# Kernel optimization log

Hardware: AMD Instinct MI355X
Metric: run time of the kernel (lower is better)

The kernel has to match this reference:

```python
import jax, jax.numpy as jnp
import numpy as np

N_QUBITS = 16
N_BLOCKS = 8
N_ADDR_QUBITS = 4  # (8).bit_length() -> min(n_qubits, bit_length)
N_HEADS = 16


def setup_inputs() -> dict:
    key = jax.random.key(0)
    ks = jax.random.split(key, 9)
    B, S, D, M, J, Q = 4, 2048, 1024, 2048, N_BLOCKS, N_QUBITS
    s = lambda d: 1.0 / np.sqrt(d)
    return {
        "query": jax.random.normal(ks[0], (B, S, D), jnp.float32),
        "W_addr": jax.random.normal(ks[1], (D, Q), jnp.float32) * s(D),
        "b_addr": jnp.zeros((Q,), jnp.float32),
        "memory": jax.random.normal(ks[2], (J, M), jnp.float32),
        "W_out": jax.random.normal(ks[3], (M, D), jnp.float32) * s(M),
        "b_out": jnp.zeros((D,), jnp.float32),
        "Wq": jax.random.normal(ks[4], (D, D), jnp.float32) * s(D),
        "bq": jnp.zeros((D,), jnp.float32),
        "Wk": jax.random.normal(ks[5], (D, D), jnp.float32) * s(D),
        "bk": jnp.zeros((D,), jnp.float32),
        "Wv": jax.random.normal(ks[6], (D, D), jnp.float32) * s(D),
        "bv": jnp.zeros((D,), jnp.float32),
        "Wo": jax.random.normal(ks[7], (D, D), jnp.float32) * s(D),
        "bo": jnp.zeros((D,), jnp.float32),
    }


def _address_weights(query, W_addr, b_addr):
    # Deterministic expectation of the per-token quantum register loop:
    # RX(theta) applied iff theta > 0 -> P(measure 1) = sin^2(theta/2), else 0.
    theta = query @ W_addr + b_addr                      # [B,S,Q]
    p1 = jnp.where(theta > 0, jnp.sin(theta * 0.5) ** 2, 0.0)
    p = p1[..., :N_ADDR_QUBITS]                          # only bit_length(J) qubits used
    bits = ((jnp.arange(N_BLOCKS)[:, None] >> jnp.arange(N_ADDR_QUBITS)[None, :]) & 1
            ).astype(query.dtype)                        # [J, Qa]
    # score[b,s,j] = sum_q [ bits*p + (1-bits)*(1-p) ]
    scores = jnp.einsum("bsq,jq->bsj", p, bits) + jnp.einsum("bsq,jq->bsj", 1.0 - p, 1.0 - bits)
    return jax.nn.softmax(scores, axis=-1)               # [B,S,J]


def reference(query, W_addr, b_addr, memory, W_out, b_out,
              Wq, bq, Wk, bk, Wv, bv, Wo, bo):
    addr = _address_weights(query, W_addr, b_addr)       # [B,S,J]
    mem_read = jnp.einsum("bsj,jm->bsm", addr, memory)   # [B,S,M]
    out = mem_read @ W_out + b_out                       # [B,S,D]

    # quantum_attention(q=k=v=out): multi-head self-attention
    B, S, D = out.shape
    hd = D // N_HEADS
    q = (out @ Wq + bq).reshape(B, S, N_HEADS, hd)
    k = (out @ Wk + bk).reshape(B, S, N_HEADS, hd)
    v = (out @ Wv + bv).reshape(B, S, N_HEADS, hd)
    att = jax.nn.softmax(jnp.einsum("bihd,bjhd->bhij", q, k) / np.sqrt(hd), axis=-1)
    ctx = jnp.einsum("bhij,bjhd->bihd", att, v).reshape(B, S, D)
    return ctx @ Wo + bo
```

## Files before the change

kernel.cpp:

```cpp
#include <hip/hip_runtime.h>

#define B_ 4
#define S_ 2048
#define D_ 1024
#define M_ 2048
#define J_ 8
#define H_ 16
#define HD_ 64
#define BH_ 64

typedef __attribute__((ext_vector_type(8))) short short8;
typedef __attribute__((ext_vector_type(4))) float f32x4;
typedef __attribute__((ext_vector_type(16))) float f32x16;

static __device__ __forceinline__ unsigned short f2bf(float x) {
  unsigned u = __float_as_uint(x);
  u = u + 0x7fffu + ((u >> 16) & 1u);
  return (unsigned short)(u >> 16);
}

static __device__ __forceinline__ unsigned cvtpk(float lo, float hi) {
  unsigned r;
  asm("v_cvt_pk_bf16_f32 %0, %1, %2" : "=v"(r) : "v"(lo), "v"(hi));
  return r;
}

static __device__ __forceinline__ void gload16(const void* g, void* l) {
  __builtin_amdgcn_global_load_lds(
      (const __attribute__((address_space(1))) unsigned*)g,
      (__attribute__((address_space(3))) unsigned*)l, 16, 0, 0);
}

__global__ __launch_bounds__(256) void k_mw_part(const float* __restrict__ memory,
                                                 const float* __restrict__ W_out,
                                                 float* __restrict__ part) {
  int nc = blockIdx.x >> 4, ks = blockIdx.x & 15;
  int t = threadIdx.x;
  int n = nc * 64 + (t & 63);
  int sub = t >> 6;
  int k0 = ks * 128 + sub * 32;
  float acc[J_];
#pragma unroll
  for (int j = 0; j < J_; ++j) acc[j] = 0.f;
  for (int k = k0; k < k0 + 32; ++k) {
    float wv = W_out[(size_t)k * D_ + n];
#pragma unroll
    for (int j = 0; j < J_; ++j) acc[j] += memory[j * M_ + k] * wv;
  }
  __shared__ float p4[4][J_][64];
#pragma unroll
  for (int j = 0; j < J_; ++j) p4[sub][j][t & 63] = acc[j];
  __syncthreads();
  if (t < 64) {
#pragma unroll
    for (int j = 0; j < J_; ++j)
      part[((size_t)ks * J_ + j) * D_ + nc * 64 + t] =
          p4[0][j][t] + p4[1][j][t] + p4[2][j][t] + p4[3][j][t];
  }
}

__global__ __launch_bounds__(256) void k_mw_red(const float* __restrict__ part,
                                                const float* __restrict__ b_out,
                                                float* __restrict__ G) {
  int id = blockIdx.x * 256 + threadIdx.x;
  int j = id >> 10, n = id & 1023;
  if (j < 8) {
    float s = 0.f;
#pragma unroll
    for (int ks = 0; ks < 16; ++ks) s += part[((size_t)ks * J_ + j) * D_ + n];
    G[j * D_ + n] = s;
  } else {
    G[8 * D_ + n] = b_out[n];
  }
}

__global__ __launch_bounds__(256) void k_mwq_part(const float* __restrict__ G,
                                                  const float* __restrict__ Wq,
                                                  const float* __restrict__ Wk,
                                                  const float* __restrict__ Wv,
                                                  float* __restrict__ partq) {
  int wi = blockIdx.x >> 6;
  int r = blockIdx.x & 63;
  int nc = r & 15, ks = r >> 4;
  const float* W = wi == 0 ? Wq : (wi == 1 ? Wk : Wv);
  int t = threadIdx.x;
  int n = nc * 64 + (t & 63);
  int sub = t >> 6;
  int k0 = ks * 256 + sub * 64;
  float acc[9];
#pragma unroll
  for (int j = 0; j < 9; ++j) acc[j] = 0.f;
  for (int k = k0; k < k0 + 64; ++k) {
    float wv = W[(size_t)k * D_ + n];
#pragma unroll
    for (int j = 0; j < 9; ++j) acc[j] += G[j * D_ + k] * wv;
  }
  __shared__ float p4[4][9][64];
#pragma unroll
  for (int j = 0; j < 9; ++j) p4[sub][j][t & 63] = acc[j];
  __syncthreads();
  if (t < 64) {
#pragma unroll
    for (int j = 0; j < 9; ++j)
      partq[(((size_t)wi * 4 + ks) * 9 + j) * D_ + nc * 64 + t] =
          p4[0][j][t] + p4[1][j][t] + p4[2][j][t] + p4[3][j][t];
  }
}

__global__ __launch_bounds__(256) void k_mwq_red(const float* __restrict__ partq,
                                                 float* __restrict__ Hq,
                                                 float* __restrict__ Hk,
                                                 float* __restrict__ Hv) {
  int id = blockIdx.x * 256 + threadIdx.x;
  int wi = id / 9216;
  int rem = id - wi * 9216;
  int j = rem >> 10, n = rem & 1023;
  float s = 0.f;
#pragma unroll
  for (int ks = 0; ks < 4; ++ks)
    s += partq[(((size_t)wi * 4 + ks) * 9 + j) * D_ + n];
  float* Hh = wi == 0 ? Hq : (wi == 1 ? Hk : Hv);
  Hh[j * D_ + n] = s;
}

__global__ __launch_bounds__(256) void k_wot(const float* __restrict__ Wo,
                                             unsigned short* __restrict__ WoT) {
  int kt = blockIdx.x, nt = blockIdx.y;
  int t = threadIdx.x;
  __shared__ float tl[64][65];
  int r = t >> 6, c = t & 63;
#pragma unroll
  for (int i = 0; i < 16; ++i) {
    int row = i * 4 + r;
    tl[row][c] = Wo[(size_t)(kt * 64 + row) * D_ + nt * 64 + c];
  }
  __syncthreads();
#pragma unroll
  for (int i = 0; i < 16; ++i) {
    int nrow = i * 4 + r;
    WoT[(size_t)(nt * 64 + nrow) * D_ + kt * 64 + c] = f2bf(tl[c][nrow]);
  }
}

__global__ __launch_bounds__(256) void k_qkv(
    const float* __restrict__ query, const float* __restrict__ W_addr,
    const float* __restrict__ b_addr, const float* __restrict__ Hq,
    const float* __restrict__ Hk, const float* __restrict__ Hv,
    const float* __restrict__ bq, const float* __restrict__ bk,
    const float* __restrict__ bv, unsigned short* __restrict__ Qg,
    unsigned short* __restrict__ Kg, unsigned short* __restrict__ Vg) {
  int w = threadIdx.x >> 6, l = threadIdx.x & 63;
  int tk = blockIdx.x * 4 + w;
  int b = tk >> 11, s = tk & (S_ - 1);
  const float* qrow = query + (size_t)tk * D_;
  float th0 = 0.f, th1 = 0.f, th2 = 0.f, th3 = 0.f;
#pragma unroll
  for (int e = 0; e < 4; ++e) {
    float4 qv = *(const float4*)(qrow + l * 16 + e * 4);
    float xs[4] = {qv.x, qv.y, qv.z, qv.w};
#pragma unroll
    for (int kk = 0; kk < 4; ++kk) {
      float4 wr = *(const float4*)(W_addr + (size_t)(l * 16 + e * 4 + kk) * 16);
      th0 += xs[kk] * wr.x;
      th1 += xs[kk] * wr.y;
      th2 += xs[kk] * wr.z;
      th3 += xs[kk] * wr.w;
    }
  }
#pragma unroll
  for (int off = 32; off; off >>= 1) {
    th0 += __shfl_xor(th0, off);
    th1 += __shfl_xor(th1, off);
    th2 += __shfl_xor(th2, off);
    th3 += __shfl_xor(th3, off);
  }
  float thv[4] = {th0 + b_addr[0], th1 + b_addr[1], th2 + b_addr[2],
                  th3 + b_addr[3]};
  float p[4];
#pragma unroll
  for (int q = 0; q < 4; ++q) {
    float sh = __sinf(thv[q] * 0.5f);
    p[q] = thv[q] > 0.f ? sh * sh : 0.f;
  }
  float sc[8];
  float mx = -1e30f;
#pragma unroll
  for (int j = 0; j < 8; ++j) {
    float v = 0.f;
#pragma unroll
    for (int q = 0; q < 4; ++q) v += ((j >> q) & 1) ? p[q] : 1.f - p[q];
    sc[j] = v;
    mx = fmaxf(mx, v);
  }
  float sum = 0.f;
#pragma unroll
  for (int j = 0; j < 8; ++j) {
    sc[j] = __expf(sc[j] - mx);
    sum += sc[j];
  }
  float inv = 1.f / sum;
  float a[8];
#pragma unroll
  for (int j = 0; j < 8; ++j) a[j] = sc[j] * inv;

  const float* Hs[3] = {Hq, Hk, Hv};
  const float* bs[3] = {bq, bk, bv};
  unsigned short* os[3] = {Qg, Kg, Vg};
#pragma unroll
  for (int k = 0; k < 4; ++k) {
    int n0 = k * 256 + l * 4;
    int hh = n0 >> 6, d = n0 & 63;
    size_t obase = ((size_t)(b * H_ + hh) * S_ + s) * HD_ + d;
#pragma unroll
    for (int wi = 0; wi < 3; ++wi) {
      const float* Hh = Hs[wi];
      float4 accv = *(const float4*)(Hh + 8 * D_ + n0);
      float4 bias = *(const float4*)(bs[wi] + n0);
      accv.x += bias.x; accv.y += bias.y; accv.z += bias.z; accv.w += bias.w;
#pragma unroll
      for (int j = 0; j < 8; ++j) {
        float4 hv = *(const float4*)(Hh + j * D_ + n0);
        accv.x += a[j] * hv.x;
        accv.y += a[j] * hv.y;
        accv.z += a[j] * hv.z;
        accv.w += a[j] * hv.w;
      }
      uint2 pk;
      pk.x = (unsigned)f2bf(accv.x) | ((unsigned)f2bf(accv.y) << 16);
      pk.y = (unsigned)f2bf(accv.z) | ((unsigned)f2bf(accv.w) << 16);
      *(uint2*)(os[wi] + obase) = pk;
    }
  }
}

__global__ __launch_bounds__(256) void k_vt(const unsigned short* __restrict__ Vg,
                                            unsigned short* __restrict__ Vtg) {
  int st = blockIdx.x & 31, bh = blockIdx.x >> 5;
  int t = threadIdx.x;
  __shared__ unsigned short tl[64][65];
  int rr = t >> 3, c8 = t & 7;
#pragma unroll
  for (int p = 0; p < 2; ++p) {
    int s = p * 32 + rr;
    uint4 v = *(const uint4*)(Vg + ((size_t)bh * S_ + st * 64 + s) * HD_ + c8 * 8);
    const unsigned short* pv = (const unsigned short*)&v;
#pragma unroll
    for (int j = 0; j < 8; ++j) tl[s][c8 * 8 + j] = pv[j];
  }
  __syncthreads();
#pragma unroll
  for (int p = 0; p < 2; ++p) {
    int d = p * 32 + rr;
    unsigned short o[8];
#pragma unroll
    for (int j = 0; j < 8; ++j) o[j] = tl[c8 * 8 + j][d];
    *(uint4*)(Vtg + ((size_t)bh * HD_ + d) * S_ + st * 64 + c8 * 8) = *(const uint4*)o;
  }
}

__global__ __launch_bounds__(512, 4) void k_attn(
    const unsigned short* __restrict__ Qg, const unsigned short* __restrict__ Kg,
    const unsigned short* __restrict__ Vtg, unsigned short* __restrict__ ctxg) {
  int id = blockIdx.x;
  int xcd = id & 7;
  int qt = (id >> 3) & 15;
  int bh = xcd * 8 + (id >> 7);
  int t = threadIdx.x;
  int w = t >> 6, l = t & 63;
  int q31 = l & 31, h = l >> 5;
  int g = w >> 2;

  __shared__ __align__(16) unsigned short lds[32768];

  int q0 = qt * 128;
  const unsigned short* qp = Qg + ((size_t)bh * S_ + q0 + (w & 3) * 32 + q31) * HD_;
  short8 qf0 = *(const short8*)(qp + 0 + h * 8);
  short8 qf1 = *(const short8*)(qp + 16 + h * 8);
  short8 qf2 = *(const short8*)(qp + 32 + h * 8);
  short8 qf3 = *(const short8*)(qp + 48 + h * 8);

  f32x16 accO0 = {}, accO1 = {};
  float lsum = 0.f;

  const unsigned short* kgb = Kg + (size_t)bh * S_ * HD_;
  const unsigned short* vtb = Vtg + (size_t)bh * HD_ * S_;
  int wg = w & 3;
  int rowK = l >> 3, gsl = l & 7;
  int srcg = gsl ^ rowK;

  {
    unsigned short* sKd = lds + g * 8192;
    unsigned short* sVd = sKd + 4096;
#pragma unroll
    for (int cc = 0; cc < 2; ++cc) {
      int c = wg * 2 + cc;
      int rr = c * 8 + rowK;
      gload16(kgb + ((size_t)(g * 1024 + rr)) * HD_ + srcg * 8, sKd + c * 512);
      gload16(vtb + (size_t)rr * S_ + g * 1024 + srcg * 8, sVd + c * 512);
    }
  }
  __syncthreads();

  const float K1 = 0.125f * 1.44269504f;
  const float M2 = 28.8539008f;

  for (int it = 0; it < 16; ++it) {
    if (it < 15) {
      int kvn = g * 1024 + (it + 1) * 64;
      unsigned short* sKd = lds + ((it + 1) & 1) * 16384 + g * 8192;
      unsigned short* sVd = sKd + 4096;
#pragma unroll
      for (int cc = 0; cc < 2; ++cc) {
        int c = wg * 2 + cc;
        int rr = c * 8 + rowK;
        gload16(kgb + (size_t)(kvn + rr) * HD_ + srcg * 8, sKd + c * 512);
        gload16(vtb + (size_t)rr * S_ + kvn + srcg * 8, sVd + c * 512);
      }
    }
    unsigned short* sK = lds + (it & 1) * 16384 + g * 8192;
    unsigned short* sVt = sK + 4096;

    f32x16 accS0 = {}, accS1 = {};
    __builtin_amdgcn_s_setprio(1);
#pragma unroll
    for (int ds = 0; ds < 4; ++ds) {
      short8 qq = ds == 0 ? qf0 : ds == 1 ? qf1 : ds == 2 ? qf2 : qf3;
      {
        int row = q31;
        int gk = (ds * 2 + h) ^ (row & 7);
        short8 kf = *(const short8*)(sK + row * 64 + gk * 8);
        accS0 = __builtin_amdgcn_mfma_f32_32x32x16_bf16(kf, qq, accS0, 0, 0, 0);
      }
      {
        int row = 32 + q31;
        int gk = (ds * 2 + h) ^ (row & 7);
        short8 kf = *(const short8*)(sK + row * 64 + gk * 8);
        accS1 = __builtin_amdgcn_mfma_f32_32x32x16_bf16(kf, qq, accS1, 0, 0, 0);
      }
    }
    __builtin_amdgcn_s_setprio(0);

    float ts = 0.f;
#pragma unroll
    for (int r = 0; r < 16; ++r) {
      float p0 = __builtin_exp2f(accS0[r] * K1 - M2);
      float p1 = __builtin_exp2f(accS1[r] * K1 - M2);
      accS0[r] = p0;
      accS1[r] = p1;
      ts += p0 + p1;
    }
    lsum += ts;

    short8 pb[4];
#pragma unroll
    for (int ks = 0; ks < 4; ++ks) {
      const int r0 = 8 * (ks & 1);
      float v0, v1, v2, v3, v4, v5, v6, v7;
      if (ks < 2) {
        v0 = accS0[r0 + 0]; v1 = accS0[r0 + 1]; v2 = accS0[r0 + 2]; v3 = accS0[r0 + 3];
        v4 = accS0[r0 + 4]; v5 = accS0[r0 + 5]; v6 = accS0[r0 + 6]; v7 = accS0[r0 + 7];
      } else {
        v0 = accS1[r0 + 0]; v1 = accS1[r0 + 1]; v2 = accS1[r0 + 2]; v3 = accS1[r0 + 3];
        v4 = accS1[r0 + 4]; v5 = accS1[r0 + 5]; v6 = accS1[r0 + 6]; v7 = accS1[r0 + 7];
      }
      unsigned X0 = cvtpk(v0, v1), X1 = cvtpk(v2, v3);
      unsigned Y0 = cvtpk(v4, v5), Y1 = cvtpk(v6, v7);
      union { unsigned u[4]; short8 s8; } uu;
#if __has_builtin(__builtin_amdgcn_permlane32_swap)
      typedef __attribute__((ext_vector_type(2))) unsigned uint2v;
      uint2v r02 = __builtin_amdgcn_permlane32_swap(X0, Y0, false, false);
      uint2v r13 = __builtin_amdgcn_permlane32_swap(X1, Y1, false, false);
      uu.u[0] = r02[0]; uu.u[1] = r13[0]; uu.u[2] = r02[1]; uu.u[3] = r13[1];
#else
      unsigned tX0 = __shfl_xor(X0, 32), tX1 = __shfl_xor(X1, 32);
      unsigned tY0 = __shfl_xor(Y0, 32), tY1 = __shfl_xor(Y1, 32);
      uu.u[0] = h ? tY0 : X0;
      uu.u[1] = h ? tY1 : X1;
      uu.u[2] = h ? Y0 : tX0;
      uu.u[3] = h ? Y1 : tX1;
#endif
      pb[ks] = uu.s8;
    }

    __builtin_amdgcn_s_setprio(1);
    {
      int row = q31;
      int rs = row & 7;
#pragma unroll
      for (int ks = 0; ks < 4; ++ks) {
        int gv = (ks * 2 + h) ^ rs;
        short8 vf = *(const short8*)(sVt + row * 64 + gv * 8);
        accO0 = __builtin_amdgcn_mfma_f32_32x32x16_bf16(vf, pb[ks], accO0, 0, 0, 0);
      }
    }
    {
      int row = 32 + q31;
      int rs = row & 7;
#pragma unroll
      for (int ks = 0; ks < 4; ++ks) {
        int gv = (ks * 2 + h) ^ rs;
        short8 vf = *(const short8*)(sVt + row * 64 + gv * 8);
        accO1 = __builtin_amdgcn_mfma_f32_32x32x16_bf16(vf, pb[ks], accO1, 0, 0, 0);
      }
    }
    __builtin_amdgcn_s_setprio(0);

    __syncthreads();
  }

  float lt = lsum + __shfl_xor(lsum, 32);

  if (g == 1) {
    unsigned* xO = (unsigned*)lds;
    int base = ((w & 3) * 64 + l) * 17;
#pragma unroll
    for (int j = 0; j < 8; ++j) xO[base + j] = cvtpk(accO0[2 * j], accO0[2 * j + 1]);
#pragma unroll
    for (int j = 0; j < 8; ++j) xO[base + 8 + j] = cvtpk(accO1[2 * j], accO1[2 * j + 1]);
    float* xml = (float*)(lds + 8704);
    if (h == 0) xml[(w & 3) * 32 + q31] = lt;
  }
  __syncthreads();
  float inv = 0.f;
  if (g == 0) {
    unsigned* xO = (unsigned*)lds;
    float* xml = (float*)(lds + 8704);
    int base = (w * 64 + l) * 17;
    inv = 1.f / (lt + xml[w * 32 + q31]);
#pragma unroll
    for (int j = 0; j < 8; ++j) {
      unsigned wd = xO[base + j];
      accO0[2 * j] += __uint_as_float(wd << 16);
      accO0[2 * j + 1] += __uint_as_float(wd & 0xffff0000u);
    }
#pragma unroll
    for (int j = 0; j < 8; ++j) {
      unsigned wd = xO[base + 8 + j];
      accO1[2 * j] += __uint_as_float(wd << 16);
      accO1[2 * j + 1] += __uint_as_float(wd & 0xffff0000u);
    }
  }
  __syncthreads();
  if (g == 0) {
    int row = w * 32 + q31;
    int swz = (q31 & 7) << 3;
#pragma unroll
    for (int r = 0; r < 16; ++r) {
      int dl = (r & 3) + 8 * (r >> 2) + 4 * h;
      lds[row * 64 + (dl ^ swz)] = f2bf(accO0[r] * inv);
      lds[row * 64 + ((32 + dl) ^ swz)] = f2bf(accO1[r] * inv);
    }
  }
  __syncthreads();
  int b = bh >> 4, head = bh & 15;
#pragma unroll
  for (int j = 0; j < 2; ++j) {
    int slot = t + j * 512;
    int row = slot >> 3, gg = slot & 7;
    uint4 vv = *(const uint4*)(lds + row * 64 + ((gg ^ (row & 7)) * 8));
    *(uint4*)(ctxg + ((size_t)(b * S_ + q0 + row)) * D_ + head * HD_ + gg * 8) = vv;
  }
}

__global__ __launch_bounds__(256) void k_out(const unsigned short* __restrict__ Ag,
                                             const unsigned short* __restrict__ Btg,
                                             const float* __restrict__ bo,
                                             float* __restrict__ out) {
  int mt = blockIdx.x;
  int nt = blockIdx.y;
  int t = threadIdx.x;
  int w = t >> 6, l = t & 63;
  int l15 = l & 15, l4 = l >> 4;
  int wr = w >> 1, wc = w & 1;
  __shared__ __align__(16) unsigned short sA[128 * 64];
  __shared__ __align__(16) unsigned short sB[128 * 64];
  f32x4 acc[4][4];
#pragma unroll
  for (int mm = 0; mm < 4; ++mm)
#pragma unroll
    for (int nn = 0; nn < 4; ++nn) acc[mm][nn] = (f32x4){0.f, 0.f, 0.f, 0.f};
  int srow = t >> 3, sc8 = t & 7;
  for (int kt = 0; kt < 16; ++kt) {
    int k0 = kt * 64;
    __syncthreads();
#pragma unroll
    for (int p = 0; p < 4; ++p) {
      int row = p * 32 + srow;
      int di = row * 64 + ((sc8 * 8) ^ ((row & 7) << 3));
      *(uint4*)(sA + di) =
          *(const uint4*)(Ag + (size_t)(mt * 128 + row) * D_ + k0 + sc8 * 8);
      *(uint4*)(sB + di) =
          *(const uint4*)(Btg + (size_t)(nt * 128 + row) * D_ + k0 + sc8 * 8);
    }
    __syncthreads();
    short8 a[4][2];
#pragma unroll
    for (int mm = 0; mm < 4; ++mm) {
      int row = wr * 64 + mm * 16 + l15;
      int sw = (row & 7) << 3;
      a[mm][0] = *(const short8*)(sA + row * 64 + ((l4 * 8) ^ sw));
      a[mm][1] = *(const short8*)(sA + row * 64 + ((32 + l4 * 8) ^ sw));
    }
#pragma unroll
    for (int nn = 0; nn < 4; ++nn) {
      int row = wc * 64 + nn * 16 + l15;
      int sw = (row & 7) << 3;
      short8 b0 = *(const short8*)(sB + row * 64 + ((l4 * 8) ^ sw));
      short8 b1 = *(const short8*)(sB + row * 64 + ((32 + l4 * 8) ^ sw));
#pragma unroll
      for (int mm = 0; mm < 4; ++mm) {
        acc[mm][nn] = __builtin_amdgcn_mfma_f32_16x16x32_bf16(a[mm][0], b0, acc[mm][nn], 0, 0, 0);
        acc[mm][nn] = __builtin_amdgcn_mfma_f32_16x16x32_bf16(a[mm][1], b1, acc[mm][nn], 0, 0, 0);
      }
    }
  }
#pragma unroll
  for (int mm = 0; mm < 4; ++mm) {
#pragma unroll
    for (int r = 0; r < 4; ++r) {
      int mrow = mt * 128 + wr * 64 + mm * 16 + l4 * 4 + r;
      float* orow = out + (size_t)mrow * D_ + nt * 128 + wc * 64;
#pragma unroll
      for (int nn = 0; nn < 4; ++nn) {
        int n = nn * 16 + l15;
        orow[n] = acc[mm][nn][r] + bo[nt * 128 + wc * 64 + n];
      }
    }
  }
}

extern "C" void kernel_launch(void* const* d_in, const int* in_sizes, int n_in,
                              void* d_out, int out_size, void* d_ws, size_t ws_size,
                              hipStream_t stream) {
  const float* query = (const float*)d_in[0];
  const float* W_addr = (const float*)d_in[1];
  const float* b_addr = (const float*)d_in[2];
  const float* memory = (const float*)d_in[3];
  const float* W_out = (const float*)d_in[4];
  const float* b_out = (const float*)d_in[5];
  const float* Wq = (const float*)d_in[6];
  const float* bq = (const float*)d_in[7];
  const float* Wk = (const float*)d_in[8];
  const float* bk = (const float*)d_in[9];
  const float* Wv = (const float*)d_in[10];
  const float* bv = (const float*)d_in[11];
  const float* Wo = (const float*)d_in[12];
  const float* bo = (const float*)d_in[13];
  float* out = (float*)d_out;

  char* ws = (char*)d_ws;
  size_t off = 0;
  auto alloc = [&](size_t bytes) {
    char* p = ws + off;
    off = (off + bytes + 255) & ~(size_t)255;
    return p;
  };
  float* G = (float*)alloc(9 * D_ * sizeof(float));
  float* HqA = (float*)alloc(9 * D_ * sizeof(float));
  float* HkA = (float*)alloc(9 * D_ * sizeof(float));
  float* HvA = (float*)alloc(9 * D_ * sizeof(float));
  float* partmw = (float*)alloc(16 * J_ * D_ * sizeof(float));
  float* partq = (float*)alloc(3 * 4 * 9 * D_ * sizeof(float));
  unsigned short* WoT = (unsigned short*)alloc((size_t)D_ * D_ * 2);
  unsigned short* Vg = (unsigned short*)alloc((size_t)BH_ * S_ * HD_ * 2);
  unsigned short* Vtg = (unsigned short*)alloc((size_t)BH_ * S_ * HD_ * 2);
  unsigned short* Qg = (unsigned short*)d_out;
  unsigned short* Kg = Qg + (size_t)BH_ * S_ * HD_;
  unsigned short* ctx = Vg;

  k_mw_part<<<256, 256, 0, stream>>>(memory, W_out, partmw);
  k_mw_red<<<36, 256, 0, stream>>>(partmw, b_out, G);
  k_mwq_part<<<192, 256, 0, stream>>>(G, Wq, Wk, Wv, partq);
  k_mwq_red<<<108, 256, 0, stream>>>(partq, HqA, HkA, HvA);
  k_wot<<<dim3(16, 16), 256, 0, stream>>>(Wo, WoT);
  k_qkv<<<B_ * S_ / 4, 256, 0, stream>>>(query, W_addr, b_addr, HqA, HkA, HvA,
                                         bq, bk, bv, Qg, Kg, Vg);
  k_vt<<<BH_ * 32, 256, 0, stream>>>(Vg, Vtg);
  k_attn<<<1024, 512, 0, stream>>>(Qg, Kg, Vtg, ctx);
  k_out<<<dim3(64, 8), 256, 0, stream>>>(ctx, WoT, bo, out);
}
```

Measured before the change: 241.0 us.

## Stage QKV projection tables in LDS as bf16, fold biases and softmax scale

Transposes W_addr for coalesced theta loads and folds the q/k/v biases into the H tables, with the attention scale and log2e pre-multiplied into Hq. k_qkv now stages all three H tables as packed bf16 in shared memory and processes 32 tokens per 512-thread block, writing 16 contiguous outputs per lane. The attention kernel initialises its score accumulators with the max offset so the per-element multiply-subtract before exp2 disappears. This trades some precision (bf16 H tables, a pre-scaled Q) for less global traffic and fewer ALU ops in both kernels.

New measurement: 484.4 us. +101.0%, slower.

```diff
diff --git a/kernel.cpp b/kernel.cpp
--- a/kernel.cpp
+++ b/kernel.cpp
@@ -12,6 +12,9 @@
 typedef __attribute__((ext_vector_type(8))) short short8;
 typedef __attribute__((ext_vector_type(4))) float f32x4;
 typedef __attribute__((ext_vector_type(16))) float f32x16;
+
+#define QSCALE 0.18033688f
+#define M2F 28.8539008f
 
 static __device__ __forceinline__ unsigned short f2bf(float x) {
   unsigned u = __float_as_uint(x);
@@ -61,7 +64,16 @@
 
 __global__ __launch_bounds__(256) void k_mw_red(const float* __restrict__ part,
                                                 const float* __restrict__ b_out,
-                                                float* __restrict__ G) {
+                                                const float* __restrict__ W_addr,
+                                                float* __restrict__ G,
+                                                float* __restrict__ WaT) {
+  if (blockIdx.x >= 36) {
+    int q = blockIdx.x - 36;
+    int c = threadIdx.x * 4;
+#pragma unroll
+    for (int e = 0; e < 4; ++e) WaT[q * D_ + c + e] = W_addr[(size_t)(c + e) * 16 + q];
+    return;
+  }
   int id = blockIdx.x * 256 + threadIdx.x;
   int j = id >> 10, n = id & 1023;
   if (j < 8) {
@@ -108,6 +120,9 @@
 }
 
 __global__ __launch_bounds__(256) void k_mwq_red(const float* __restrict__ partq,
+                                                 const float* __restrict__ bq,
+                                                 const float* __restrict__ bk,
+                                                 const float* __restrict__ bv,
                                                  float* __restrict__ Hq,
                                                  float* __restrict__ Hk,
                                                  float* __restrict__ Hv) {
@@ -119,6 +134,8 @@
 #pragma unroll
   for (int ks = 0; ks < 4; ++ks)
     s += partq[(((size_t)wi * 4 + ks) * 9 + j) * D_ + n];
+  if (j == 8) s += wi == 0 ? bq[n] : (wi == 1 ? bk[n] : bv[n]);
+  if (wi == 0) s *= QSCALE;
   float* Hh = wi == 0 ? Hq : (wi == 1 ? Hk : Hv);
   Hh[j * D_ + n] = s;
 }
@@ -142,93 +159,110 @@
   }
 }
 
-__global__ __launch_bounds__(256) void k_qkv(
-    const float* __restrict__ query, const float* __restrict__ W_addr,
+__global__ __launch_bounds__(512) void k_qkv(
+    const float* __restrict__ query, const float* __restrict__ WaT,
     const float* __restrict__ b_addr, const float* __restrict__ Hq,
     const float* __restrict__ Hk, const float* __restrict__ Hv,
-    const float* __restrict__ bq, const float* __restrict__ bk,
-    const float* __restrict__ bv, unsigned short* __restrict__ Qg,
-    unsigned short* __restrict__ Kg, unsigned short* __restrict__ Vg) {
-  int w = threadIdx.x >> 6, l = threadIdx.x & 63;
-  int tk = blockIdx.x * 4 + w;
-  int b = tk >> 11, s = tk & (S_ - 1);
-  const float* qrow = query + (size_t)tk * D_;
-  float th0 = 0.f, th1 = 0.f, th2 = 0.f, th3 = 0.f;
-#pragma unroll
-  for (int e = 0; e < 4; ++e) {
-    float4 qv = *(const float4*)(qrow + l * 16 + e * 4);
-    float xs[4] = {qv.x, qv.y, qv.z, qv.w};
-#pragma unroll
-    for (int kk = 0; kk < 4; ++kk) {
-      float4 wr = *(const float4*)(W_addr + (size_t)(l * 16 + e * 4 + kk) * 16);
-      th0 += xs[kk] * wr.x;
-      th1 += xs[kk] * wr.y;
-      th2 += xs[kk] * wr.z;
-      th3 += xs[kk] * wr.w;
-    }
-  }
-#pragma unroll
-  for (int off = 32; off; off >>= 1) {
-    th0 += __shfl_xor(th0, off);
-    th1 += __shfl_xor(th1, off);
-    th2 += __shfl_xor(th2, off);
-    th3 += __shfl_xor(th3, off);
-  }
-  float thv[4] = {th0 + b_addr[0], th1 + b_addr[1], th2 + b_addr[2],
-                  th3 + b_addr[3]};
-  float p[4];
-#pragma unroll
-  for (int q = 0; q < 4; ++q) {
-    float sh = __sinf(thv[q] * 0.5f);
-    p[q] = thv[q] > 0.f ? sh * sh : 0.f;
-  }
-  float sc[8];
-  float mx = -1e30f;
-#pragma unroll
-  for (int j = 0; j < 8; ++j) {
-    float v = 0.f;
-#pragma unroll
-    for (int q = 0; q < 4; ++q) v += ((j >> q) & 1) ? p[q] : 1.f - p[q];
-    sc[j] = v;
-    mx = fmaxf(mx, v);
-  }
-  float sum = 0.f;
-#pragma unroll
-  for (int j = 0; j < 8; ++j) {
-    sc[j] = __expf(sc[j] - mx);
-    sum += sc[j];
-  }
-  float inv = 1.f / sum;
-  float a[8];
-#pragma unroll
-  for (int j = 0; j < 8; ++j) a[j] = sc[j] * inv;
-
+    unsigned short* __restrict__ Qg, unsigned short* __restrict__ Kg,
+    unsigned short* __restrict__ Vg) {
+  __shared__ unsigned HL[13824];
+  int t = threadIdx.x;
   const float* Hs[3] = {Hq, Hk, Hv};
-  const float* bs[3] = {bq, bk, bv};
-  unsigned short* os[3] = {Qg, Kg, Vg};
-#pragma unroll
-  for (int k = 0; k < 4; ++k) {
-    int n0 = k * 256 + l * 4;
-    int hh = n0 >> 6, d = n0 & 63;
-    size_t obase = ((size_t)(b * H_ + hh) * S_ + s) * HD_ + d;
-#pragma unroll
-    for (int wi = 0; wi < 3; ++wi) {
-      const float* Hh = Hs[wi];
-      float4 accv = *(const float4*)(Hh + 8 * D_ + n0);
-      float4 bias = *(const float4*)(bs[wi] + n0);
-      accv.x += bias.x; accv.y += bias.y; accv.z += bias.z; accv.w += bias.w;
+#pragma unroll
+  for (int i = 0; i < 27; ++i) {
+    int fid = i * 512 + t;
+    int mat = fid / 4608;
+    int rem = fid - mat * 4608;
+    int row = rem >> 9, cp = rem & 511;
+    float2 v = *(const float2*)(Hs[mat] + (size_t)row * D_ + cp * 2);
+    HL[fid] = cvtpk(v.x, v.y);
+  }
+  __syncthreads();
+
+  int w = t >> 6, l = t & 63;
+  float ba0 = b_addr[0], ba1 = b_addr[1], ba2 = b_addr[2], ba3 = b_addr[3];
+  for (int rd = 0; rd < 4; ++rd) {
+    int tk = blockIdx.x * 32 + rd * 8 + w;
+    int b = tk >> 11, s = tk & (S_ - 1);
+    const float* qrow = query + (size_t)tk * D_;
+    float th0 = 0.f, th1 = 0.f, th2 = 0.f, th3 = 0.f;
+#pragma unroll
+    for (int e = 0; e < 4; ++e) {
+      float4 qv = *(const float4*)(qrow + l * 16 + e * 4);
+      float4 w0 = *(const float4*)(WaT + 0 * D_ + l * 16 + e * 4);
+      float4 w1 = *(const float4*)(WaT + 1 * D_ + l * 16 + e * 4);
+      float4 w2 = *(const float4*)(WaT + 2 * D_ + l * 16 + e * 4);
+      float4 w3 = *(const float4*)(WaT + 3 * D_ + l * 16 + e * 4);
+      th0 += qv.x * w0.x + qv.y * w0.y + qv.z * w0.z + qv.w * w0.w;
+      th1 += qv.x * w1.x + qv.y * w1.y + qv.z * w1.z + qv.w * w1.w;
+      th2 += qv.x * w2.x + qv.y * w2.y + qv.z * w2.z + qv.w * w2.w;
+      th3 += qv.x * w3.x + qv.y * w3.y + qv.z * w3.z + qv.w * w3.w;
+    }
+#pragma unroll
+    for (int off = 32; off; off >>= 1) {
+      th0 += __shfl_xor(th0, off);
+      th1 += __shfl_xor(th1, off);
+      th2 += __shfl_xor(th2, off);
+      th3 += __shfl_xor(th3, off);
+    }
+    float thv[4] = {th0 + ba0, th1 + ba1, th2 + ba2, th3 + ba3};
+    float p[4];
+#pragma unroll
+    for (int q = 0; q < 4; ++q) {
+      float sh = __sinf(thv[q] * 0.5f);
+      p[q] = thv[q] > 0.f ? sh * sh : 0.f;
+    }
+    float sc[8];
+    float mx = -1e30f;
+#pragma unroll
+    for (int j = 0; j < 8; ++j) {
+      float v = 0.f;
+#pragma unroll
+      for (int q = 0; q < 4; ++q) v += ((j >> q) & 1) ? p[q] : 1.f - p[q];
+      sc[j] = v;
+      mx = fmaxf(mx, v);
+    }
+    float sum = 0.f;
+#pragma unroll
+    for (int j = 0; j < 8; ++j) {
+      sc[j] = __expf(sc[j] - mx);
+      sum += sc[j];
+    }
+    float inv = 1.f / sum;
+    float a[8];
+#pragma unroll
+    for (int j = 0; j < 8; ++j) a[j] = sc[j] * inv;
+
+    int head = l >> 2, d0 = (l & 3) * 16;
+    size_t obase = ((size_t)(b * H_ + head) * S_ + s) * HD_ + d0;
+    unsigned short* os[3] = {Qg, Kg, Vg};
+#pragma unroll
+    for (int mat = 0; mat < 3; ++mat) {
+      const unsigned* hb = HL + mat * 4608;
+      float acc[16];
+#pragma unroll
+      for (int c = 0; c < 8; ++c) {
+        unsigned wd = hb[8 * 512 + 8 * l + c];
+        acc[2 * c] = __uint_as_float(wd << 16);
+        acc[2 * c + 1] = __uint_as_float(wd & 0xffff0000u);
+      }
 #pragma unroll
       for (int j = 0; j < 8; ++j) {
-        float4 hv = *(const float4*)(Hh + j * D_ + n0);
-        accv.x += a[j] * hv.x;
-        accv.y += a[j] * hv.y;
-        accv.z += a[j] * hv.z;
-        accv.w += a[j] * hv.w;
-      }
-      uint2 pk;
-      pk.x = (unsigned)f2bf(accv.x) | ((unsigned)f2bf(accv.y) << 16);
-      pk.y = (unsigned)f2bf(accv.z) | ((unsigned)f2bf(accv.w) << 16);
-      *(uint2*)(os[wi] + obase) = pk;
+        float aj = a[j];
+        const unsigned* hr = hb + j * 512 + 8 * l;
+#pragma unroll
+        for (int c = 0; c < 8; ++c) {
+          unsigned wd = hr[c];
+          acc[2 * c] += aj * __uint_as_float(wd << 16);
+          acc[2 * c + 1] += aj * __uint_as_float(wd & 0xffff0000u);
+        }
+      }
+      unsigned ow[8];
+#pragma unroll
+      for (int c = 0; c < 8; ++c) ow[c] = (unsigned)f2bf(acc[2 * c]) |
+                                          ((unsigned)f2bf(acc[2 * c + 1]) << 16);
+      *(uint4*)(os[mat] + obase) = *(const uint4*)&ow[0];
+      *(uint4*)(os[mat] + obase + 8) = *(const uint4*)&ow[4];
     }
   }
 }
@@ -301,9 +335,6 @@
   }
   __syncthreads();
 
-  const float K1 = 0.125f * 1.44269504f;
-  const float M2 = 28.8539008f;
-
   for (int it = 0; it < 16; ++it) {
     if (it < 15) {
       int kvn = g * 1024 + (it + 1) * 64;
@@ -320,7 +351,9 @@
     unsigned short* sK = lds + (it & 1) * 16384 + g * 8192;
     unsigned short* sVt = sK + 4096;
 
-    f32x16 accS0 = {}, accS1 = {};
+    f32x16 accS0, accS1;
+#pragma unroll
+    for (int r = 0; r < 16; ++r) { accS0[r] = -M2F; accS1[r] = -M2F; }
     __builtin_amdgcn_s_setprio(1);
 #pragma unroll
     for (int ds = 0; ds < 4; ++ds) {
@@ -343,8 +376,8 @@
     float ts = 0.f;
 #pragma unroll
     for (int r = 0; r < 16; ++r) {
-      float p0 = __builtin_exp2f(accS0[r] * K1 - M2);
-      float p1 = __builtin_exp2f(accS1[r] * K1 - M2);
+      float p0 = __builtin_exp2f(accS0[r]);
+      float p1 = __builtin_exp2f(accS1[r]);
       accS0[r] = p0;
       accS1[r] = p1;
       ts += p0 + p1;
@@ -559,6 +592,7 @@
   float* HqA = (float*)alloc(9 * D_ * sizeof(float));
   float* HkA = (float*)alloc(9 * D_ * sizeof(float));
   float* HvA = (float*)alloc(9 * D_ * sizeof(float));
+  float* WaT = (float*)alloc(4 * D_ * sizeof(float));
   float* partmw = (float*)alloc(16 * J_ * D_ * sizeof(float));
   float* partq = (float*)alloc(3 * 4 * 9 * D_ * sizeof(float));
   unsigned short* WoT = (unsigned short*)alloc((size_t)D_ * D_ * 2);
@@ -569,12 +603,11 @@
   unsigned short* ctx = Vg;
 
   k_mw_part<<<256, 256, 0, stream>>>(memory, W_out, partmw);
-  k_mw_red<<<36, 256, 0, stream>>>(partmw, b_out, G);
+  k_mw_red<<<40, 256, 0, stream>>>(partmw, b_out, W_addr, G, WaT);
   k_mwq_part<<<192, 256, 0, stream>>>(G, Wq, Wk, Wv, partq);
-  k_mwq_red<<<108, 256, 0, stream>>>(partq, HqA, HkA, HvA);
+  k_mwq_red<<<108, 256, 0, stream>>>(partq, bq, bk, bv, HqA, HkA, HvA);
   k_wot<<<dim3(16, 16), 256, 0, stream>>>(Wo, WoT);
-  k_qkv<<<B_ * S_ / 4, 256, 0, stream>>>(query, W_addr, b_addr, HqA, HkA, HvA,
-                                         bq, bk, bv, Qg, Kg, Vg);
+  k_qkv<<<256, 512, 0, stream>>>(query, WaT, b_addr, HqA, HkA, HvA, Qg, Kg, Vg);
   k_vt<<<BH_ * 32, 256, 0, stream>>>(Vg, Vtg);
   k_attn<<<1024, 512, 0, stream>>>(Qg, Kg, Vtg, ctx);
   k_out<<<dim3(64, 8), 256, 0, stream>>>(ctx, WoT, bo, out);
```

## Fold softmax scale and bias into H tables, transpose W_addr for coalesced loads

Applied to the files above, without the earlier changes.

Folds the q/k/v biases and the attention softmax scale (1/sqrt(hd)·log2e) into the precomputed Hq/Hk/Hv tables, and folds the fixed max offset into the MFMA accumulator's initial value. This removes the per-element multiply-subtract before exp2 in the attention inner loop and the bias loads in k_qkv. It also transposes the first four columns of W_addr into a small buffer, so the address-projection loads in k_qkv are coalesced float4 reads instead of strided ones. Scaling Q before bf16 rounding changes numerics slightly.

Measured after the change: 259.4 us. 1.08x slower.

```diff
diff --git a/kernel.cpp b/kernel.cpp
--- a/kernel.cpp
+++ b/kernel.cpp
@@ -12,6 +12,9 @@
 typedef __attribute__((ext_vector_type(8))) short short8;
 typedef __attribute__((ext_vector_type(4))) float f32x4;
 typedef __attribute__((ext_vector_type(16))) float f32x16;
+
+#define QSCALE 0.18033688f
+#define M2F 28.8539008f
 
 static __device__ __forceinline__ unsigned short f2bf(float x) {
   unsigned u = __float_as_uint(x);
@@ -61,7 +64,16 @@
 
 __global__ __launch_bounds__(256) void k_mw_red(const float* __restrict__ part,
                                                 const float* __restrict__ b_out,
-                                                float* __restrict__ G) {
+                                                const float* __restrict__ W_addr,
+                                                float* __restrict__ G,
+                                                float* __restrict__ WaT) {
+  if (blockIdx.x >= 36) {
+    int q = blockIdx.x - 36;
+    int c = threadIdx.x * 4;
+#pragma unroll
+    for (int e = 0; e < 4; ++e) WaT[q * D_ + c + e] = W_addr[(size_t)(c + e) * 16 + q];
+    return;
+  }
   int id = blockIdx.x * 256 + threadIdx.x;
   int j = id >> 10, n = id & 1023;
   if (j < 8) {
@@ -108,6 +120,9 @@
 }
 
 __global__ __launch_bounds__(256) void k_mwq_red(const float* __restrict__ partq,
+                                                 const float* __restrict__ bq,
+                                                 const float* __restrict__ bk,
+                                                 const float* __restrict__ bv,
                                                  float* __restrict__ Hq,
                                                  float* __restrict__ Hk,
                                                  float* __restrict__ Hv) {
@@ -119,6 +134,8 @@
 #pragma unroll
   for (int ks = 0; ks < 4; ++ks)
     s += partq[(((size_t)wi * 4 + ks) * 9 + j) * D_ + n];
+  if (j == 8) s += wi == 0 ? bq[n] : (wi == 1 ? bk[n] : bv[n]);
+  if (wi == 0) s *= QSCALE;
   float* Hh = wi == 0 ? Hq : (wi == 1 ? Hk : Hv);
   Hh[j * D_ + n] = s;
 }
@@ -143,12 +160,11 @@
 }
 
 __global__ __launch_bounds__(256) void k_qkv(
-    const float* __restrict__ query, const float* __restrict__ W_addr,
+    const float* __restrict__ query, const float* __restrict__ WaT,
     const float* __restrict__ b_addr, const float* __restrict__ Hq,
     const float* __restrict__ Hk, const float* __restrict__ Hv,
-    const float* __restrict__ bq, const float* __restrict__ bk,
-    const float* __restrict__ bv, unsigned short* __restrict__ Qg,
-    unsigned short* __restrict__ Kg, unsigned short* __restrict__ Vg) {
+    unsigned short* __restrict__ Qg, unsigned short* __restrict__ Kg,
+    unsigned short* __restrict__ Vg) {
   int w = threadIdx.x >> 6, l = threadIdx.x & 63;
   int tk = blockIdx.x * 4 + w;
   int b = tk >> 11, s = tk & (S_ - 1);
@@ -156,16 +172,15 @@
   float th0 = 0.f, th1 = 0.f, th2 = 0.f, th3 = 0.f;
 #pragma unroll
   for (int e = 0; e < 4; ++e) {
-    float4 qv = *(const float4*)(qrow + l * 16 + e * 4);
-    float xs[4] = {qv.x, qv.y, qv.z, qv.w};
-#pragma unroll
-    for (int kk = 0; kk < 4; ++kk) {
-      float4 wr = *(const float4*)(W_addr + (size_t)(l * 16 + e * 4 + kk) * 16);
-      th0 += xs[kk] * wr.x;
-      th1 += xs[kk] * wr.y;
-      th2 += xs[kk] * wr.z;
-      th3 += xs[kk] * wr.w;
-    }
+    float4 qv = *(const float4*)(qrow + e * 256 + l * 4);
+    float4 w0 = *(const float4*)(WaT + 0 * D_ + e * 256 + l * 4);
+    float4 w1 = *(const float4*)(WaT + 1 * D_ + e * 256 + l * 4);
+    float4 w2 = *(const float4*)(WaT + 2 * D_ + e * 256 + l * 4);
+    float4 w3 = *(const float4*)(WaT + 3 * D_ + e * 256 + l * 4);
+    th0 += qv.x * w0.x + qv.y * w0.y + qv.z * w0.z + qv.w * w0.w;
+    th1 += qv.x * w1.x + qv.y * w1.y + qv.z * w1.z + qv.w * w1.w;
+    th2 += qv.x * w2.x + qv.y * w2.y + qv.z * w2.z + qv.w * w2.w;
+    th3 += qv.x * w3.x + qv.y * w3.y + qv.z * w3.z + qv.w * w3.w;
   }
 #pragma unroll
   for (int off = 32; off; off >>= 1) {
@@ -204,7 +219,6 @@
   for (int j = 0; j < 8; ++j) a[j] = sc[j] * inv;
 
   const float* Hs[3] = {Hq, Hk, Hv};
-  const float* bs[3] = {bq, bk, bv};
   unsigned short* os[3] = {Qg, Kg, Vg};
 #pragma unroll
   for (int k = 0; k < 4; ++k) {
@@ -215,8 +229,6 @@
     for (int wi = 0; wi < 3; ++wi) {
       const float* Hh = Hs[wi];
       float4 accv = *(const float4*)(Hh + 8 * D_ + n0);
-      float4 bias = *(const float4*)(bs[wi] + n0);
-      accv.x += bias.x; accv.y += bias.y; accv.z += bias.z; accv.w += bias.w;
 #pragma unroll
       for (int j = 0; j < 8; ++j) {
         float4 hv = *(const float4*)(Hh + j * D_ + n0);
@@ -301,9 +313,6 @@
   }
   __syncthreads();
 
-  const float K1 = 0.125f * 1.44269504f;
-  const float M2 = 28.8539008f;
-
   for (int it = 0; it < 16; ++it) {
     if (it < 15) {
       int kvn = g * 1024 + (it + 1) * 64;
@@ -320,7 +329,9 @@
     unsigned short* sK = lds + (it & 1) * 16384 + g * 8192;
     unsigned short* sVt = sK + 4096;
 
-    f32x16 accS0 = {}, accS1 = {};
+    f32x16 accS0, accS1;
+#pragma unroll
+    for (int r = 0; r < 16; ++r) { accS0[r] = -M2F; accS1[r] = -M2F; }
     __builtin_amdgcn_s_setprio(1);
 #pragma unroll
     for (int ds = 0; ds < 4; ++ds) {
@@ -343,8 +354,8 @@
     float ts = 0.f;
 #pragma unroll
     for (int r = 0; r < 16; ++r) {
-      float p0 = __builtin_exp2f(accS0[r] * K1 - M2);
-      float p1 = __builtin_exp2f(accS1[r] * K1 - M2);
+      float p0 = __builtin_exp2f(accS0[r]);
+      float p1 = __builtin_exp2f(accS1[r]);
       accS0[r] = p0;
       accS1[r] = p1;
       ts += p0 + p1;
@@ -559,6 +570,7 @@
   float* HqA = (float*)alloc(9 * D_ * sizeof(float));
   float* HkA = (float*)alloc(9 * D_ * sizeof(float));
   float* HvA = (float*)alloc(9 * D_ * sizeof(float));
+  float* WaT = (float*)alloc(4 * D_ * sizeof(float));
   float* partmw = (float*)alloc(16 * J_ * D_ * sizeof(float));
   float* partq = (float*)alloc(3 * 4 * 9 * D_ * sizeof(float));
   unsigned short* WoT = (unsigned short*)alloc((size_t)D_ * D_ * 2);
@@ -569,12 +581,12 @@
   unsigned short* ctx = Vg;
 
   k_mw_part<<<256, 256, 0, stream>>>(memory, W_out, partmw);
-  k_mw_red<<<36, 256, 0, stream>>>(partmw, b_out, G);
+  k_mw_red<<<40, 256, 0, stream>>>(partmw, b_out, W_addr, G, WaT);
   k_mwq_part<<<192, 256, 0, stream>>>(G, Wq, Wk, Wv, partq);
-  k_mwq_red<<<108, 256, 0, stream>>>(partq, HqA, HkA, HvA);
+  k_mwq_red<<<108, 256, 0, stream>>>(partq, bq, bk, bv, HqA, HkA, HvA);
   k_wot<<<dim3(16, 16), 256, 0, stream>>>(Wo, WoT);
-  k_qkv<<<B_ * S_ / 4, 256, 0, stream>>>(query, W_addr, b_addr, HqA, HkA, HvA,
-                                         bq, bk, bv, Qg, Kg, Vg);
+  k_qkv<<<B_ * S_ / 4, 256, 0, stream>>>(query, WaT, b_addr, HqA, HkA, HvA,
+                                         Qg, Kg, Vg);
   k_vt<<<BH_ * 32, 256, 0, stream>>>(Vg, Vtg);
   k_attn<<<1024, 512, 0, stream>>>(Qg, Kg, Vtg, ctx);
   k_out<<<dim3(64, 8), 256, 0, stream>>>(ctx, WoT, bo, out);
```
